# Optimization experiments

Hardware: AMD Instinct MI355X
Metric: run time of the kernel (lower is better)

The kernel has to match this reference:

```python
import jax, jax.numpy as jnp
import numpy as np

K = 1024
T = 16384
P = 2          # number of lags
N_STAGES = 2   # len(s_list)
EDGE_P = 0.005 # edge density -> avg degree ~5


def setup_inputs() -> dict:
    key = jax.random.key(0)
    kX, kA, ka, kb0, kb1 = jax.random.split(key, 5)
    X = jax.random.normal(kX, (K, T), dtype=jnp.float32)
    # sparse symmetric 0/1 adjacency, zero diagonal
    U = jax.random.uniform(kA, (K, K))
    Ab = (U < EDGE_P)
    Ab = (Ab | Ab.T) & ~jnp.eye(K, dtype=bool)
    A = Ab.astype(jnp.float32)
    alpha = jax.random.normal(ka, (P,), dtype=jnp.float32)
    beta0 = jax.random.normal(kb0, (P,), dtype=jnp.float32)
    beta1 = jax.random.normal(kb1, (P,), dtype=jnp.float32)
    return {"X": X, "A": A, "alpha": alpha, "beta0": beta0, "beta1": beta1}


def _stage_avg_matrices(A):
    """M[r] averages over nodes at shortest-path distance exactly r+1 (rows with
    no stage-r neighbors are all-zero, matching the `if neighbors:` guard)."""
    Ab = A > 0.5
    Af = Ab.astype(jnp.float32)
    reach_prev = jnp.eye(A.shape[0], dtype=bool)  # distance <= 0
    Ms = []
    for _ in range(N_STAGES):
        reach = reach_prev | ((reach_prev.astype(jnp.float32) @ Af) > 0.5)
        exact = reach & ~reach_prev                     # distance == r+1
        exact_f = exact.astype(jnp.float32)
        deg = exact_f.sum(axis=1, keepdims=True)        # (K, 1)
        M = exact_f / jnp.maximum(deg, 1.0)             # zero rows stay zero
        Ms.append(M)
        reach_prev = reach
    return Ms


def reference(X, A, alpha, beta0, beta1):
    K_, T_ = X.shape
    betas = [beta0, beta1]
    Ms = _stage_avg_matrices(A)
    # one dense aggregation per stage over ALL time steps, then slice lags
    MXs = [M @ X for M in Ms]                           # each (K, T)
    Y = jnp.zeros((K_, T_ - P), dtype=X.dtype)
    for lag in range(1, P + 1):
        sl = slice(P - lag, T_ - lag)
        Y = Y + alpha[lag - 1] * X[:, sl]
        for stage in range(N_STAGES):
            Y = Y + betas[stage][lag - 1] * MXs[stage][:, sl]
    return Y
```

## Files before the change

kernel.cpp:

```cpp
#include <hip/hip_runtime.h>

typedef float fx4 __attribute__((ext_vector_type(4)));
typedef short s16x8 __attribute__((ext_vector_type(8)));
typedef __bf16 bfx8 __attribute__((ext_vector_type(8)));

#define KN 1024
#define TT 16384
#define NOUT 16382
#define NKT 32

#define APK_OFF 67108864u

__device__ __forceinline__ unsigned short f2bf(float f) {
  return __builtin_bit_cast(unsigned short, (__bf16)f);
}

__device__ __forceinline__ void gll16(const void* g, void* l) {
  __builtin_amdgcn_global_load_lds(
      (const __attribute__((address_space(1))) void*)g,
      (__attribute__((address_space(3))) void*)l, 16, 0, 0);
}

__global__ __launch_bounds__(256) void k_masks(const float* __restrict__ A,
                                               unsigned* __restrict__ B1) {
  int k = blockIdx.x;
  int tid = threadIdx.x;
  int wv = tid >> 6, lane = tid & 63;
  for (int i = 0; i < 4; ++i) {
    int n = i * 256 + wv * 64 + lane;
    bool bit = (A[(size_t)k * KN + n] > 0.5f) && (n != k);
    unsigned long long m = __ballot(bit);
    if (lane == 0) {
      B1[k * 32 + i * 8 + wv * 2]     = (unsigned)m;
      B1[k * 32 + i * 8 + wv * 2 + 1] = (unsigned)(m >> 32);
    }
  }
}

__global__ __launch_bounds__(256) void k_weights(const unsigned* __restrict__ B1,
                                                 const float* __restrict__ alpha,
                                                 const float* __restrict__ beta0,
                                                 const float* __restrict__ beta1,
                                                 unsigned short* __restrict__ Wc) {
  __shared__ unsigned reach[32];
  __shared__ unsigned ex2[32];
  __shared__ unsigned short list[1056];
  __shared__ int nl;
  int k = blockIdx.x, tid = threadIdx.x;
  if (tid == 0) nl = 0;
  if (tid < 32) {
    unsigned r = B1[k * 32 + tid];
    if (tid == (k >> 5)) r |= 1u << (k & 31);
    reach[tid] = r;
    ex2[tid] = 0;
  }
  __syncthreads();
  for (int m = tid; m < KN; m += 256)
    if ((reach[m >> 5] >> (m & 31)) & 1) {
      int i = atomicAdd(&nl, 1);
      list[i] = (unsigned short)m;
    }
  __syncthreads();
  int n2 = nl;
  for (int i = 0; i < n2; ++i) {
    int m = list[i];
    if (tid < 32) ex2[tid] |= B1[m * 32 + tid];
  }
  __syncthreads();
  if (tid < 32) ex2[tid] &= ~reach[tid];
  __syncthreads();
  int d1 = 0, d2 = 0;
  for (int w = 0; w < 32; ++w) { d1 += __popc(reach[w]); d2 += __popc(ex2[w]); }
  d1 -= 1;
  float rd1 = 1.0f / fmaxf((float)d1, 1.0f);
  float rd2 = 1.0f / fmaxf((float)d2, 1.0f);
  float c00 = beta0[0] * rd1, c01 = beta0[1] * rd1;
  float c10 = beta1[0] * rd2, c11 = beta1[1] * rd2;
  float a0 = alpha[0], a1 = alpha[1];
  int mb = k >> 8, rloc = k & 255;
  for (int q = 0; q < 4; ++q) {
    int n = tid * 4 + q;
    bool in1 = (((reach[n >> 5] >> (n & 31)) & 1) != 0) && (n != k);
    bool in2 = ((ex2[n >> 5] >> (n & 31)) & 1) != 0;
    float v0 = (in1 ? c00 : 0.f) + (in2 ? c10 : 0.f) + (n == k ? a0 : 0.f);
    float v1 = (in1 ? c01 : 0.f) + (in2 ? c11 : 0.f) + (n == k ? a1 : 0.f);
    int kt = n >> 5, qk = (n >> 4) & 1, kb = (n >> 2) & 3, ii = (n & 3) * 2;
    size_t idx = ((((size_t)(mb * 32 + kt) * 2 + qk) * 4 + kb) * 256 + rloc) * 8 + ii;
    unsigned pair = (unsigned)f2bf(v0) | ((unsigned)f2bf(v1) << 16);
    *reinterpret_cast<unsigned*>(Wc + idx) = pair;
  }
}

__global__ __launch_bounds__(256) void k_pack_x2(const float* __restrict__ X,
                                                 unsigned short* __restrict__ Bpk) {
  int G = blockIdx.x * 256 + threadIdx.x;
  int col = G & 255;
  int kb  = (G >> 8) & 3;
  int qk  = (G >> 10) & 1;
  int kt  = (G >> 11) & 31;
  int jb  = G >> 16;
  int j   = jb * 256 + col;
  int mbase = kt * 32 + qk * 16 + kb * 4;
  unsigned v[4];
#pragma unroll
  for (int p = 0; p < 4; ++p) {
    int m = mbase + p;
    int j1 = j + 1;
    float f0 = (j1 < TT) ? X[(size_t)m * TT + j1] : 0.0f;
    float f1 = X[(size_t)m * TT + j];
    v[p] = (unsigned)f2bf(f0) | ((unsigned)f2bf(f1) << 16);
  }
  uint4 w; w.x = v[0]; w.y = v[1]; w.z = v[2]; w.w = v[3];
  *reinterpret_cast<uint4*>(Bpk + (size_t)G * 8) = w;
}

__global__ __launch_bounds__(512, 2) void k_gemm(const char* __restrict__ Apk,
                                                 const char* __restrict__ Bpk,
                                                 float* __restrict__ Y) {
  __shared__ char lds[131072];
  int bid = blockIdx.x;
  int swz = (bid & 7) * 32 + (bid >> 3);
  int jb = swz >> 2, mb = swz & 3;
  int tid = threadIdx.x;
  int lane = tid & 63, wv = tid >> 6;
  int wm = wv >> 2, wn = wv & 3;
  int kb = lane >> 4, ml = lane & 15;
  const char* Asrc = Apk + (size_t)mb * (NKT * 2 * 16384);
  const char* Bsrc = Bpk + (size_t)jb * (NKT * 2 * 16384);

  fx4 acc[2][4][4];
#pragma unroll
  for (int q = 0; q < 2; ++q)
#pragma unroll
    for (int a = 0; a < 4; ++a)
#pragma unroll
      for (int b = 0; b < 4; ++b) acc[q][a][b] = (fx4){0.f, 0.f, 0.f, 0.f};

  auto stage_half = [&](int tile, int isB, int qh) {
    char* dst = lds + (tile & 1) * 65536 + isB * 32768 + qh * 16384;
    const char* src = (isB ? Bsrc : Asrc) + ((size_t)(tile & (NKT - 1)) * 2 + qh) * 16384;
    gll16(src + tid * 16, dst + tid * 16);
    gll16(src + (size_t)(tid + 512) * 16, dst + (tid + 512) * 16);
  };

#define READ_A(dst, t, qk, qm)                                                      \
  do {                                                                              \
    const char* Ah_ = lds + ((t) & 1) * 65536 + (qk) * 16384;                       \
    _Pragma("unroll") for (int mf = 0; mf < 4; ++mf)                                \
      dst[mf] = *(const s16x8*)(Ah_ +                                               \
          (size_t)(kb * 256 + wm * 128 + (qm) * 64 + mf * 16 + ml) * 16);           \
  } while (0)
#define READ_B(dst, t, qk)                                                          \
  do {                                                                              \
    const char* Bh_ = lds + ((t) & 1) * 65536 + 32768 + (qk) * 16384;               \
    _Pragma("unroll") for (int nf = 0; nf < 4; ++nf)                                \
      dst[nf] = *(const s16x8*)(Bh_ +                                               \
          (size_t)(kb * 256 + wn * 64 + nf * 16 + ml) * 16);                        \
  } while (0)
#define MFMA16(acc_, a_, b_)                                                        \
  do {                                                                              \
    __builtin_amdgcn_sched_barrier(0);                                              \
    __builtin_amdgcn_s_setprio(1);                                                  \
    _Pragma("unroll") for (int mf = 0; mf < 4; ++mf)                                \
      _Pragma("unroll") for (int nf = 0; nf < 4; ++nf)                              \
        acc_[mf][nf] = __builtin_amdgcn_mfma_f32_16x16x32_bf16(                     \
            __builtin_bit_cast(bfx8, a_[mf]), __builtin_bit_cast(bfx8, b_[nf]),     \
            acc_[mf][nf], 0, 0, 0);                                                 \
    __builtin_amdgcn_s_setprio(0);                                                  \
    __builtin_amdgcn_sched_barrier(0);                                              \
  } while (0)

  s16x8 aA[4], aB[4], bA[4], bB[4];

  stage_half(0, 0, 0); stage_half(0, 1, 0);
  stage_half(0, 0, 1); stage_half(0, 1, 1);
  stage_half(1, 0, 0); stage_half(1, 1, 0);
  asm volatile("s_waitcnt vmcnt(8)" ::: "memory");
  __builtin_amdgcn_s_barrier();
  READ_A(aA, 0, 0, 0);
  READ_B(bA, 0, 0);

  for (int kt = 0; kt < NKT; ++kt) {
    READ_A(aB, kt, 0, 1);
    stage_half(kt + 1, 0, 1);
    MFMA16(acc[0], aA, bA);
    asm volatile("s_waitcnt vmcnt(6)" ::: "memory");
    __builtin_amdgcn_s_barrier();
    READ_A(aA, kt, 1, 0);
    READ_B(bB, kt, 1);
    stage_half(kt + 1, 1, 1);
    MFMA16(acc[1], aB, bA);
    __builtin_amdgcn_s_barrier();
    READ_A(aB, kt, 1, 1);
    stage_half(kt + 2, 0, 0);
    MFMA16(acc[0], aA, bB);
    asm volatile("s_waitcnt vmcnt(6)" ::: "memory");
    __builtin_amdgcn_s_barrier();
    READ_A(aA, kt + 1, 0, 0);
    READ_B(bA, kt + 1, 0);
    stage_half(kt + 2, 1, 0);
    MFMA16(acc[1], aB, bB);
    __builtin_amdgcn_s_barrier();
  }
  asm volatile("s_waitcnt vmcnt(0)" ::: "memory");

  int c0 = jb * 256 + wn * 64;
  int r0 = mb * 256 + wm * 128;
#pragma unroll
  for (int qm = 0; qm < 2; ++qm)
#pragma unroll
    for (int mf = 0; mf < 4; ++mf)
#pragma unroll
      for (int nf = 0; nf < 4; ++nf) {
        int c = c0 + nf * 16 + ml;
        if (c < NOUT) {
          int r = r0 + qm * 64 + mf * 16 + (lane >> 4) * 4;
#pragma unroll
          for (int i = 0; i < 4; ++i)
            Y[(size_t)(r + i) * NOUT + c] = acc[qm][mf][nf][i];
        }
      }
#undef READ_A
#undef READ_B
#undef MFMA16
}

extern "C" void kernel_launch(void* const* d_in, const int* in_sizes, int n_in,
                              void* d_out, int out_size, void* d_ws, size_t ws_size,
                              hipStream_t stream) {
  const float* X     = (const float*)d_in[0];
  const float* A     = (const float*)d_in[1];
  const float* alpha = (const float*)d_in[2];
  const float* beta0 = (const float*)d_in[3];
  const float* beta1 = (const float*)d_in[4];
  float* Y = (float*)d_out;
  char* ws = (char*)d_ws;
  char* Bpk = ws;
  char* Apk = ws + APK_OFF;
  unsigned* B1 = (unsigned*)ws;

  k_masks<<<dim3(1024), dim3(256), 0, stream>>>(A, B1);
  k_weights<<<dim3(1024), dim3(256), 0, stream>>>(B1, alpha, beta0, beta1,
                                                  (unsigned short*)Apk);
  k_pack_x2<<<dim3(16384), dim3(256), 0, stream>>>(X, (unsigned short*)Bpk);
  k_gemm<<<dim3(256), dim3(512), 0, stream>>>(Apk, Bpk, Y);
}
```

Baseline: 93.83 us.

## Use 4 waves with 128x128 per-wave tiles in GEMM kernel

Restructures the GEMM block from 8 waves (each 128x64 output) to 4 waves, each computing a 128x128 tile of 8x8 MFMA fragments. This raises the ratio of MFMA work to LDS fragment reads and halves the barrier participants, while each thread now issues 8 global-to-LDS loads per stage. The cost is a 256-register accumulator array per thread, which risks spills or very low occupancy, and half as many waves available to hide latency.

```diff
diff --git a/kernel.cpp b/kernel.cpp
--- a/kernel.cpp
+++ b/kernel.cpp
@@ -114,7 +114,7 @@
   *reinterpret_cast<uint4*>(Bpk + (size_t)G * 8) = w;
 }
 
-__global__ __launch_bounds__(512, 2) void k_gemm(const char* __restrict__ Apk,
+__global__ __launch_bounds__(256, 1) void k_gemm(const char* __restrict__ Apk,
                                                  const char* __restrict__ Bpk,
                                                  float* __restrict__ Y) {
   __shared__ char lds[131072];
@@ -123,106 +123,93 @@
   int jb = swz >> 2, mb = swz & 3;
   int tid = threadIdx.x;
   int lane = tid & 63, wv = tid >> 6;
-  int wm = wv >> 2, wn = wv & 3;
+  int wm = wv >> 1, wn = wv & 1;
   int kb = lane >> 4, ml = lane & 15;
   const char* Asrc = Apk + (size_t)mb * (NKT * 2 * 16384);
   const char* Bsrc = Bpk + (size_t)jb * (NKT * 2 * 16384);
-
-  fx4 acc[2][4][4];
-#pragma unroll
-  for (int q = 0; q < 2; ++q)
-#pragma unroll
-    for (int a = 0; a < 4; ++a)
-#pragma unroll
-      for (int b = 0; b < 4; ++b) acc[q][a][b] = (fx4){0.f, 0.f, 0.f, 0.f};
-
-  auto stage_half = [&](int tile, int isB, int qh) {
-    char* dst = lds + (tile & 1) * 65536 + isB * 32768 + qh * 16384;
-    const char* src = (isB ? Bsrc : Asrc) + ((size_t)(tile & (NKT - 1)) * 2 + qh) * 16384;
-    gll16(src + tid * 16, dst + tid * 16);
-    gll16(src + (size_t)(tid + 512) * 16, dst + (tid + 512) * 16);
+  int aoff = (kb * 256 + wm * 128 + ml) * 16;
+  int boff = (kb * 256 + wn * 128 + ml) * 16;
+
+  fx4 acc[8][8];
+#pragma unroll
+  for (int a = 0; a < 8; ++a)
+#pragma unroll
+    for (int b = 0; b < 8; ++b) acc[a][b] = (fx4){0.f, 0.f, 0.f, 0.f};
+
+  auto stage_pair = [&](int t, int qh) {
+    int buf = t & 1, ts = t & (NKT - 1);
+    char* dA = lds + buf * 65536 + qh * 16384;
+    char* dB = dA + 32768;
+    const char* sA = Asrc + ((size_t)ts * 2 + qh) * 16384;
+    const char* sB = Bsrc + ((size_t)ts * 2 + qh) * 16384;
+#pragma unroll
+    for (int u = 0; u < 4; ++u)
+      gll16(sA + tid * 16 + u * 4096, dA + tid * 16 + u * 4096);
+#pragma unroll
+    for (int u = 0; u < 4; ++u)
+      gll16(sB + tid * 16 + u * 4096, dB + tid * 16 + u * 4096);
   };
 
-#define READ_A(dst, t, qk, qm)                                                      \
+#define READ_AB(adst, bdst, t, qk)                                                  \
   do {                                                                              \
     const char* Ah_ = lds + ((t) & 1) * 65536 + (qk) * 16384;                       \
-    _Pragma("unroll") for (int mf = 0; mf < 4; ++mf)                                \
-      dst[mf] = *(const s16x8*)(Ah_ +                                               \
-          (size_t)(kb * 256 + wm * 128 + (qm) * 64 + mf * 16 + ml) * 16);           \
+    const char* Bh_ = Ah_ + 32768;                                                  \
+    _Pragma("unroll") for (int mf = 0; mf < 8; ++mf)                                \
+      adst[mf] = *(const s16x8*)(Ah_ + aoff + mf * 256);                            \
+    _Pragma("unroll") for (int nf = 0; nf < 8; ++nf)                                \
+      bdst[nf] = *(const s16x8*)(Bh_ + boff + nf * 256);                            \
   } while (0)
-#define READ_B(dst, t, qk)                                                          \
-  do {                                                                              \
-    const char* Bh_ = lds + ((t) & 1) * 65536 + 32768 + (qk) * 16384;               \
-    _Pragma("unroll") for (int nf = 0; nf < 4; ++nf)                                \
-      dst[nf] = *(const s16x8*)(Bh_ +                                               \
-          (size_t)(kb * 256 + wn * 64 + nf * 16 + ml) * 16);                        \
-  } while (0)
-#define MFMA16(acc_, a_, b_)                                                        \
+
+#define MFMA64(a_, b_)                                                              \
   do {                                                                              \
     __builtin_amdgcn_sched_barrier(0);                                              \
     __builtin_amdgcn_s_setprio(1);                                                  \
-    _Pragma("unroll") for (int mf = 0; mf < 4; ++mf)                                \
-      _Pragma("unroll") for (int nf = 0; nf < 4; ++nf)                              \
-        acc_[mf][nf] = __builtin_amdgcn_mfma_f32_16x16x32_bf16(                     \
+    _Pragma("unroll") for (int mf = 0; mf < 8; ++mf)                                \
+      _Pragma("unroll") for (int nf = 0; nf < 8; ++nf)                              \
+        acc[mf][nf] = __builtin_amdgcn_mfma_f32_16x16x32_bf16(                      \
             __builtin_bit_cast(bfx8, a_[mf]), __builtin_bit_cast(bfx8, b_[nf]),     \
-            acc_[mf][nf], 0, 0, 0);                                                 \
+            acc[mf][nf], 0, 0, 0);                                                  \
     __builtin_amdgcn_s_setprio(0);                                                  \
     __builtin_amdgcn_sched_barrier(0);                                              \
   } while (0)
 
-  s16x8 aA[4], aB[4], bA[4], bB[4];
-
-  stage_half(0, 0, 0); stage_half(0, 1, 0);
-  stage_half(0, 0, 1); stage_half(0, 1, 1);
-  stage_half(1, 0, 0); stage_half(1, 1, 0);
+  s16x8 aC[8], bC[8], aN[8], bN[8];
+
+  stage_pair(0, 0); stage_pair(0, 1); stage_pair(1, 0);
   asm volatile("s_waitcnt vmcnt(8)" ::: "memory");
   __builtin_amdgcn_s_barrier();
-  READ_A(aA, 0, 0, 0);
-  READ_B(bA, 0, 0);
+  READ_AB(aC, bC, 0, 0);
 
   for (int kt = 0; kt < NKT; ++kt) {
-    READ_A(aB, kt, 0, 1);
-    stage_half(kt + 1, 0, 1);
-    MFMA16(acc[0], aA, bA);
-    asm volatile("s_waitcnt vmcnt(6)" ::: "memory");
+    READ_AB(aN, bN, kt, 1);
+    stage_pair(kt + 1, 1);
+    MFMA64(aC, bC);
+    asm volatile("s_waitcnt vmcnt(8)" ::: "memory");
     __builtin_amdgcn_s_barrier();
-    READ_A(aA, kt, 1, 0);
-    READ_B(bB, kt, 1);
-    stage_half(kt + 1, 1, 1);
-    MFMA16(acc[1], aB, bA);
+    READ_AB(aC, bC, kt + 1, 0);
+    stage_pair(kt + 2, 0);
+    MFMA64(aN, bN);
+    asm volatile("s_waitcnt vmcnt(8)" ::: "memory");
     __builtin_amdgcn_s_barrier();
-    READ_A(aB, kt, 1, 1);
-    stage_half(kt + 2, 0, 0);
-    MFMA16(acc[0], aA, bB);
-    asm volatile("s_waitcnt vmcnt(6)" ::: "memory");
-    __builtin_amdgcn_s_barrier();
-    READ_A(aA, kt + 1, 0, 0);
-    READ_B(bA, kt + 1, 0);
-    stage_half(kt + 2, 1, 0);
-    MFMA16(acc[1], aB, bB);
-    __builtin_amdgcn_s_barrier();
   }
   asm volatile("s_waitcnt vmcnt(0)" ::: "memory");
 
-  int c0 = jb * 256 + wn * 64;
+  int c0 = jb * 256 + wn * 128;
   int r0 = mb * 256 + wm * 128;
 #pragma unroll
-  for (int qm = 0; qm < 2; ++qm)
-#pragma unroll
-    for (int mf = 0; mf < 4; ++mf)
-#pragma unroll
-      for (int nf = 0; nf < 4; ++nf) {
-        int c = c0 + nf * 16 + ml;
-        if (c < NOUT) {
-          int r = r0 + qm * 64 + mf * 16 + (lane >> 4) * 4;
-#pragma unroll
-          for (int i = 0; i < 4; ++i)
-            Y[(size_t)(r + i) * NOUT + c] = acc[qm][mf][nf][i];
-        }
+  for (int mf = 0; mf < 8; ++mf)
+#pragma unroll
+    for (int nf = 0; nf < 8; ++nf) {
+      int c = c0 + nf * 16 + ml;
+      if (c < NOUT) {
+        int r = r0 + mf * 16 + (lane >> 4) * 4;
+#pragma unroll
+        for (int i = 0; i < 4; ++i)
+          Y[(size_t)(r + i) * NOUT + c] = acc[mf][nf][i];
       }
-#undef READ_A
-#undef READ_B
-#undef MFMA16
+    }
+#undef READ_AB
+#undef MFMA64
 }
 
 extern "C" void kernel_launch(void* const* d_in, const int* in_sizes, int n_in,
@@ -243,5 +230,5 @@
   k_weights<<<dim3(1024), dim3(256), 0, stream>>>(B1, alpha, beta0, beta1,
                                                   (unsigned short*)Apk);
   k_pack_x2<<<dim3(16384), dim3(256), 0, stream>>>(X, (unsigned short*)Bpk);
-  k_gemm<<<dim3(256), dim3(512), 0, stream>>>(Apk, Bpk, Y);
-}
+  k_gemm<<<dim3(256), dim3(256), 0, stream>>>(Apk, Bpk, Y);
+}
```

Result: slower. 123.7 us (+31.9%).

## Load A operand directly from global into registers, stage only B in LDS

Applied to the files above, without the earlier changes.

Repacks the coefficient matrix so each lane's 16-byte fragment is contiguous in global memory, then has the GEMM load A fragments straight into registers instead of staging them through LDS. Only B is double-buffered in LDS, which halves LDS use to 64KB and removes the A-side LDS writes and reads. In exchange each wave now issues direct global/L2 loads for A every sub-step, with the pipeline's waitcnt schedule rewritten to match. This risks exposing global latency on the MFMA critical path.

```diff
diff --git a/kernel.cpp b/kernel.cpp
--- a/kernel.cpp
+++ b/kernel.cpp
@@ -77,7 +77,7 @@
   float c00 = beta0[0] * rd1, c01 = beta0[1] * rd1;
   float c10 = beta1[0] * rd2, c11 = beta1[1] * rd2;
   float a0 = alpha[0], a1 = alpha[1];
-  int mb = k >> 8, rloc = k & 255;
+  int mb = k >> 8, rg = (k & 255) >> 4, rl = k & 15;
   for (int q = 0; q < 4; ++q) {
     int n = tid * 4 + q;
     bool in1 = (((reach[n >> 5] >> (n & 31)) & 1) != 0) && (n != k);
@@ -85,7 +85,7 @@
     float v0 = (in1 ? c00 : 0.f) + (in2 ? c10 : 0.f) + (n == k ? a0 : 0.f);
     float v1 = (in1 ? c01 : 0.f) + (in2 ? c11 : 0.f) + (n == k ? a1 : 0.f);
     int kt = n >> 5, qk = (n >> 4) & 1, kb = (n >> 2) & 3, ii = (n & 3) * 2;
-    size_t idx = ((((size_t)(mb * 32 + kt) * 2 + qk) * 4 + kb) * 256 + rloc) * 8 + ii;
+    size_t idx = (((((size_t)(mb * 32 + kt) * 2 + qk) * 16 + rg) * 4 + kb) * 16 + rl) * 8 + ii;
     unsigned pair = (unsigned)f2bf(v0) | ((unsigned)f2bf(v1) << 16);
     *reinterpret_cast<unsigned*>(Wc + idx) = pair;
   }
@@ -117,7 +117,7 @@
 __global__ __launch_bounds__(512, 2) void k_gemm(const char* __restrict__ Apk,
                                                  const char* __restrict__ Bpk,
                                                  float* __restrict__ Y) {
-  __shared__ char lds[131072];
+  __shared__ char lds[65536];
   int bid = blockIdx.x;
   int swz = (bid & 7) * 32 + (bid >> 3);
   int jb = swz >> 2, mb = swz & 3;
@@ -125,37 +125,38 @@
   int lane = tid & 63, wv = tid >> 6;
   int wm = wv >> 2, wn = wv & 3;
   int kb = lane >> 4, ml = lane & 15;
-  const char* Asrc = Apk + (size_t)mb * (NKT * 2 * 16384);
-  const char* Bsrc = Bpk + (size_t)jb * (NKT * 2 * 16384);
-
-  fx4 acc[2][4][4];
-#pragma unroll
-  for (int q = 0; q < 2; ++q)
-#pragma unroll
-    for (int a = 0; a < 4; ++a)
-#pragma unroll
-      for (int b = 0; b < 4; ++b) acc[q][a][b] = (fx4){0.f, 0.f, 0.f, 0.f};
-
-  auto stage_half = [&](int tile, int isB, int qh) {
-    char* dst = lds + (tile & 1) * 65536 + isB * 32768 + qh * 16384;
-    const char* src = (isB ? Bsrc : Asrc) + ((size_t)(tile & (NKT - 1)) * 2 + qh) * 16384;
+  const char* Asrc = Apk + (size_t)mb * 1048576 + wm * 8192 + kb * 256 + ml * 16;
+  const char* Bsrc = Bpk + (size_t)jb * 1048576;
+  int bofs = kb * 4096 + (wn * 64 + ml) * 16;
+
+  fx4 acc0[4][4], acc1[4][4];
+#pragma unroll
+  for (int a = 0; a < 4; ++a)
+#pragma unroll
+    for (int b = 0; b < 4; ++b) {
+      acc0[a][b] = (fx4){0.f, 0.f, 0.f, 0.f};
+      acc1[a][b] = (fx4){0.f, 0.f, 0.f, 0.f};
+    }
+
+  auto stage_h = [&](int t, int qh) {
+    char* dst = lds + (t & 1) * 32768 + qh * 16384;
+    const char* src = Bsrc + ((size_t)(t & (NKT - 1)) * 2 + qh) * 16384;
     gll16(src + tid * 16, dst + tid * 16);
-    gll16(src + (size_t)(tid + 512) * 16, dst + (tid + 512) * 16);
+    gll16(src + tid * 16 + 8192, dst + tid * 16 + 8192);
   };
 
-#define READ_A(dst, t, qk, qm)                                                      \
+#define LOAD_A(dst, t, qk, mh)                                                      \
   do {                                                                              \
-    const char* Ah_ = lds + ((t) & 1) * 65536 + (qk) * 16384;                       \
+    const char* Ag_ = Asrc + ((size_t)((t) & (NKT - 1))) * 32768 + (qk) * 16384 +   \
+                      (mh) * 4096;                                                  \
     _Pragma("unroll") for (int mf = 0; mf < 4; ++mf)                                \
-      dst[mf] = *(const s16x8*)(Ah_ +                                               \
-          (size_t)(kb * 256 + wm * 128 + (qm) * 64 + mf * 16 + ml) * 16);           \
+      dst[mf] = *(const s16x8*)(Ag_ + mf * 1024);                                   \
   } while (0)
 #define READ_B(dst, t, qk)                                                          \
   do {                                                                              \
-    const char* Bh_ = lds + ((t) & 1) * 65536 + 32768 + (qk) * 16384;               \
+    const char* Bh_ = lds + ((t) & 1) * 32768 + (qk) * 16384;                       \
     _Pragma("unroll") for (int nf = 0; nf < 4; ++nf)                                \
-      dst[nf] = *(const s16x8*)(Bh_ +                                               \
-          (size_t)(kb * 256 + wn * 64 + nf * 16 + ml) * 16);                        \
+      dst[nf] = *(const s16x8*)(Bh_ + bofs + nf * 256);                             \
   } while (0)
 #define MFMA16(acc_, a_, b_)                                                        \
   do {                                                                              \
@@ -170,36 +171,34 @@
     __builtin_amdgcn_sched_barrier(0);                                              \
   } while (0)
 
-  s16x8 aA[4], aB[4], bA[4], bB[4];
-
-  stage_half(0, 0, 0); stage_half(0, 1, 0);
-  stage_half(0, 0, 1); stage_half(0, 1, 1);
-  stage_half(1, 0, 0); stage_half(1, 1, 0);
-  asm volatile("s_waitcnt vmcnt(8)" ::: "memory");
+  s16x8 aC[4], aN[4], bC[4], bD[4];
+
+  stage_h(0, 0);
+  LOAD_A(aC, 0, 0, 0);
+  stage_h(0, 1);
+  asm volatile("s_waitcnt vmcnt(6)" ::: "memory");
   __builtin_amdgcn_s_barrier();
-  READ_A(aA, 0, 0, 0);
-  READ_B(bA, 0, 0);
 
   for (int kt = 0; kt < NKT; ++kt) {
-    READ_A(aB, kt, 0, 1);
-    stage_half(kt + 1, 0, 1);
-    MFMA16(acc[0], aA, bA);
-    asm volatile("s_waitcnt vmcnt(6)" ::: "memory");
-    __builtin_amdgcn_s_barrier();
-    READ_A(aA, kt, 1, 0);
-    READ_B(bB, kt, 1);
-    stage_half(kt + 1, 1, 1);
-    MFMA16(acc[1], aB, bA);
-    __builtin_amdgcn_s_barrier();
-    READ_A(aB, kt, 1, 1);
-    stage_half(kt + 2, 0, 0);
-    MFMA16(acc[0], aA, bB);
-    asm volatile("s_waitcnt vmcnt(6)" ::: "memory");
-    __builtin_amdgcn_s_barrier();
-    READ_A(aA, kt + 1, 0, 0);
-    READ_B(bA, kt + 1, 0);
-    stage_half(kt + 2, 1, 0);
-    MFMA16(acc[1], aB, bB);
+    READ_B(bC, kt, 0);
+    LOAD_A(aN, kt, 0, 1);
+    asm volatile("s_waitcnt vmcnt(6)" ::: "memory");
+    MFMA16(acc0, aC, bC);
+    __builtin_amdgcn_s_barrier();
+    LOAD_A(aC, kt, 1, 0);
+    stage_h(kt + 1, 0);
+    asm volatile("s_waitcnt vmcnt(6)" ::: "memory");
+    MFMA16(acc1, aN, bC);
+    __builtin_amdgcn_s_barrier();
+    READ_B(bD, kt, 1);
+    LOAD_A(aN, kt, 1, 1);
+    asm volatile("s_waitcnt vmcnt(6)" ::: "memory");
+    MFMA16(acc0, aC, bD);
+    __builtin_amdgcn_s_barrier();
+    LOAD_A(aC, kt + 1, 0, 0);
+    stage_h(kt + 1, 1);
+    asm volatile("s_waitcnt vmcnt(6)" ::: "memory");
+    MFMA16(acc1, aN, bD);
     __builtin_amdgcn_s_barrier();
   }
   asm volatile("s_waitcnt vmcnt(0)" ::: "memory");
@@ -207,20 +206,21 @@
   int c0 = jb * 256 + wn * 64;
   int r0 = mb * 256 + wm * 128;
 #pragma unroll
-  for (int qm = 0; qm < 2; ++qm)
+  for (int mh = 0; mh < 2; ++mh)
 #pragma unroll
     for (int mf = 0; mf < 4; ++mf)
 #pragma unroll
       for (int nf = 0; nf < 4; ++nf) {
         int c = c0 + nf * 16 + ml;
         if (c < NOUT) {
-          int r = r0 + qm * 64 + mf * 16 + (lane >> 4) * 4;
+          int r = r0 + mh * 64 + mf * 16 + (lane >> 4) * 4;
+          fx4 v = mh ? acc1[mf][nf] : acc0[mf][nf];
 #pragma unroll
           for (int i = 0; i < 4; ++i)
-            Y[(size_t)(r + i) * NOUT + c] = acc[qm][mf][nf][i];
+            Y[(size_t)(r + i) * NOUT + c] = v[i];
         }
       }
-#undef READ_A
+#undef LOAD_A
 #undef READ_B
 #undef MFMA16
 }
```

Result: slower. 119.5 us (+27.4%).
